# Optimization experiments

Hardware: AMD Instinct MI355X
Metric: run time of the kernel (lower is better)

## Reference

```python
import jax, jax.numpy as jnp
import numpy as np

NEG_SLOPE = 0.01  # F.leaky_relu default


def gcn_layer(h_in, W, b, src, dst, deg_inv_sqrt, n_nodes):
    # GCNConv: linear transform, then symmetric-normalized sum aggregation
    # with self-loops (PyG gcn_norm with add_self_loops=True).
    h = h_in @ W                                   # [N, F_out]
    norm = deg_inv_sqrt[src] * deg_inv_sqrt[dst]   # [E]
    agg = jax.ops.segment_sum(norm[:, None] * h[src], dst, num_segments=n_nodes)
    agg = agg + (deg_inv_sqrt * deg_inv_sqrt)[:, None] * h  # self-loop term (norm = 1/deg)
    return agg + b


def setup_inputs() -> dict:
    key = jax.random.key(0)
    ks = jax.random.split(key, 10)
    N, E = 100000, 3200000
    F_in, H, C = 512, 256, 64
    x = jax.random.normal(ks[0], (N, F_in), dtype=jnp.float32)
    edge_index = jax.random.randint(ks[1], (2, E), 0, N, dtype=jnp.int32)
    dims = [(F_in, H), (H, H), (H, H), (H, C)]
    params = {}
    for i, (fi, fo) in enumerate(dims):
        scale = (1.0 / fi) ** 0.5
        params[f"W{i}"] = jax.random.normal(ks[2 + i], (fi, fo), dtype=jnp.float32) * scale
        params[f"b{i}"] = jnp.zeros((fo,), dtype=jnp.float32)
    return {"x": x, "edge_index": edge_index, **params}


def reference(x, edge_index, W0, b0, W1, b1, W2, b2, W3, b3):
    N = x.shape[0]
    src, dst = edge_index[0], edge_index[1]
    # degree including self-loop (edge weights all 1)
    deg = jax.ops.segment_sum(jnp.ones_like(src, dtype=x.dtype), dst, num_segments=N) + 1.0
    deg_inv_sqrt = jax.lax.rsqrt(deg)
    Ws = [W0, W1, W2, W3]
    bs = [b0, b1, b2, b3]
    h = x
    for i in range(4):
        h = gcn_layer(h, Ws[i], bs[i], src, dst, deg_inv_sqrt, N)
        if i != 3:
            h = jax.nn.leaky_relu(h, NEG_SLOPE)
    return jax.nn.softmax(h, axis=1)
```

## Files before the change

kernel.cpp:

```cpp
#include <hip/hip_runtime.h>
#include <hip/hip_fp16.h>


#define NEG_SLOPE 0.01f

typedef __attribute__((ext_vector_type(8))) _Float16 f16x8;
typedef __attribute__((ext_vector_type(4))) float f32x4;

__device__ inline f16x8 f16x8_zero() {
    f16x8 v;
#pragma unroll
    for (int q = 0; q < 8; ++q) v[q] = (_Float16)0.f;
    return v;
}

__global__ void k_degree(const int* __restrict__ dst, int* __restrict__ cnt, int E) {
    int i = blockIdx.x * 256 + threadIdx.x;
    if (i < E) atomicAdd(&cnt[dst[i]], 1);
}

__global__ void k_dis(const int* __restrict__ cnt, float* __restrict__ dis, int N) {
    int i = blockIdx.x * 256 + threadIdx.x;
    if (i < N) dis[i] = rsqrtf((float)cnt[i] + 1.0f);
}

__global__ void k_scan1(const int* __restrict__ cnt, int* __restrict__ excl,
                        int* __restrict__ partials, int n) {
    __shared__ int tmp[1024];
    int tid = threadIdx.x;
    int i = blockIdx.x * 1024 + tid;
    int v = (i < n) ? cnt[i] : 0;
    tmp[tid] = v;
    __syncthreads();
    for (int off = 1; off < 1024; off <<= 1) {
        int t = (tid >= off) ? tmp[tid - off] : 0;
        __syncthreads();
        tmp[tid] += t;
        __syncthreads();
    }
    if (i < n) excl[i] = tmp[tid] - v;
    if (tid == 1023) partials[blockIdx.x] = tmp[tid];
}

__global__ void k_scan2(int* __restrict__ partials, int n) {
    __shared__ int tmp[1024];
    int tid = threadIdx.x;
    int v = (tid < n) ? partials[tid] : 0;
    tmp[tid] = v;
    __syncthreads();
    for (int off = 1; off < 1024; off <<= 1) {
        int t = (tid >= off) ? tmp[tid - off] : 0;
        __syncthreads();
        tmp[tid] += t;
        __syncthreads();
    }
    if (tid < n) partials[tid] = tmp[tid] - v;
}

__global__ void k_scan3(int* __restrict__ row_ptr, const int* __restrict__ partials,
                        int n, int E) {
    int i = blockIdx.x * 256 + threadIdx.x;
    if (i < n) row_ptr[i] = row_ptr[i] + partials[i >> 10];
    if (i == n) row_ptr[n] = E;
}

__global__ void k_init_bcur(const int* __restrict__ row_ptr, int* __restrict__ bcur,
                            int nbuk) {
    int b = blockIdx.x * 256 + threadIdx.x;
    if (b < nbuk) bcur[b * 16] = row_ptr[b << 7];
}

__global__ void k_bucket_fill(const int* __restrict__ src, const int* __restrict__ dst,
                              int* __restrict__ bcur, int* __restrict__ bpool, int E) {
    int i = blockIdx.x * 256 + threadIdx.x;
    if (i < E) {
        int s = src[i], d = dst[i];
        int b = d >> 7;
        int p = atomicAdd(&bcur[b * 16], 1);
        bpool[p] = (s << 7) | (d & 127);
    }
}

__global__ __launch_bounds__(256) void k_place(const int* __restrict__ bpool,
                                               const int* __restrict__ row_ptr,
                                               int* __restrict__ csr, int N) {
    __shared__ int cur[128];
    int b = blockIdx.x;
    int n0 = b << 7;
    int nn = min(128, N - n0);
    int tid = threadIdx.x;
    if (tid < nn) cur[tid] = row_ptr[n0 + tid];
    __syncthreads();
    int lo = row_ptr[n0];
    int hi = row_ptr[n0 + nn];
    for (int i = lo + tid; i < hi; i += 256) {
        int e = bpool[i];
        int p = atomicAdd(&cur[e & 127], 1);
        csr[p] = e >> 7;
    }
}

__global__ void k_convW(const float* __restrict__ W, _Float16* __restrict__ Wt,
                        int K, int Nf) {
    int gid = blockIdx.x * 256 + threadIdx.x;
    if (gid < K * Nf) {
        int n = gid / K, k = gid - n * K;
        Wt[gid] = (_Float16)W[(size_t)k * Nf + n];
    }
}

template <int BN, bool A_HALF, bool OUT_HALF>
__global__ __launch_bounds__(256) void k_gemm_mfma(const void* __restrict__ Ap,
                                                   const _Float16* __restrict__ Bt,
                                                   void* __restrict__ Cp,
                                                   const float* __restrict__ rowscale,
                                                   int M, int K, int Nf) {
    constexpr int BM = 128, BK = 32;
    constexpr int WAVES_N = (BN == 128) ? 2 : 1;
    constexpr int WAVES_M = 4 / WAVES_N;
    constexpr int WM = BM / (WAVES_M * 16);
    constexpr int WN = BN / (WAVES_N * 16);
    constexpr int LDK = BK + 8;
    __shared__ _Float16 As[BM][LDK];
    __shared__ _Float16 Bs[BN][LDK];

    const int tid = threadIdx.x;
    const int ln = tid & 63, wv = tid >> 6;
    const int wm = wv / WAVES_N, wn = wv % WAVES_N;
    const int rowq = wm * WM * 16, colq = wn * WN * 16;
    const int rowBase = blockIdx.x * BM;
    const int colBase = blockIdx.y * BN;
    const int l15 = ln & 15, lq = ln >> 4;

    f32x4 acc[WM][WN];
#pragma unroll
    for (int i = 0; i < WM; ++i)
#pragma unroll
        for (int j = 0; j < WN; ++j) {
            acc[i][j][0] = 0.f; acc[i][j][1] = 0.f;
            acc[i][j][2] = 0.f; acc[i][j][3] = 0.f;
        }

    constexpr int ASL2 = (BM * BK / 8) / 256;
    constexpr int BSL2 = (BN * BK / 8) / 256;

    for (int kt = 0; kt < K; kt += BK) {
        f16x8 aL[ASL2];
        float4 aF[ASL2][2];
#pragma unroll
        for (int s2 = 0; s2 < ASL2; ++s2) {
            int s = tid + s2 * 256;
            int r = s >> 2, k0 = (s & 3) * 8;
            int gr = rowBase + r;
            if constexpr (A_HALF) {
                aL[s2] = (gr < M)
                    ? *(const f16x8*)((const _Float16*)Ap + (size_t)gr * K + kt + k0)
                    : f16x8_zero();
            } else {
                if (gr < M) {
                    const float* ap = (const float*)Ap + (size_t)gr * K + kt + k0;
                    aF[s2][0] = *(const float4*)ap;
                    aF[s2][1] = *(const float4*)(ap + 4);
                } else {
                    aF[s2][0] = make_float4(0.f, 0.f, 0.f, 0.f);
                    aF[s2][1] = make_float4(0.f, 0.f, 0.f, 0.f);
                }
            }
        }
        f16x8 bL[BSL2];
#pragma unroll
        for (int s2 = 0; s2 < BSL2; ++s2) {
            int s = tid + s2 * 256;
            int n = s >> 2, k0 = (s & 3) * 8;
            bL[s2] = *(const f16x8*)&Bt[(size_t)(colBase + n) * K + kt + k0];
        }
        __syncthreads();
#pragma unroll
        for (int s2 = 0; s2 < ASL2; ++s2) {
            int s = tid + s2 * 256;
            int r = s >> 2, k0 = (s & 3) * 8;
            if constexpr (A_HALF) {
                *(f16x8*)&As[r][k0] = aL[s2];
            } else {
                f16x8 h;
                h[0] = (_Float16)aF[s2][0].x; h[1] = (_Float16)aF[s2][0].y;
                h[2] = (_Float16)aF[s2][0].z; h[3] = (_Float16)aF[s2][0].w;
                h[4] = (_Float16)aF[s2][1].x; h[5] = (_Float16)aF[s2][1].y;
                h[6] = (_Float16)aF[s2][1].z; h[7] = (_Float16)aF[s2][1].w;
                *(f16x8*)&As[r][k0] = h;
            }
        }
#pragma unroll
        for (int s2 = 0; s2 < BSL2; ++s2) {
            int s = tid + s2 * 256;
            int n = s >> 2, k0 = (s & 3) * 8;
            *(f16x8*)&Bs[n][k0] = bL[s2];
        }
        __syncthreads();
        f16x8 af[WM], bf[WN];
#pragma unroll
        for (int i = 0; i < WM; ++i)
            af[i] = *(const f16x8*)&As[rowq + i * 16 + l15][lq * 8];
#pragma unroll
        for (int j = 0; j < WN; ++j)
            bf[j] = *(const f16x8*)&Bs[colq + j * 16 + l15][lq * 8];
#pragma unroll
        for (int i = 0; i < WM; ++i)
#pragma unroll
            for (int j = 0; j < WN; ++j)
                acc[i][j] = __builtin_amdgcn_mfma_f32_16x16x32_f16(af[i], bf[j],
                                                                   acc[i][j], 0, 0, 0);
    }

#pragma unroll
    for (int i = 0; i < WM; ++i) {
#pragma unroll
        for (int r = 0; r < 4; ++r) {
            int row = rowBase + rowq + i * 16 + lq * 4 + r;
            if (row < M) {
                float rs = rowscale[row];
#pragma unroll
                for (int j = 0; j < WN; ++j) {
                    int col = colBase + colq + j * 16 + l15;
                    float v = rs * acc[i][j][r];
                    if constexpr (OUT_HALF)
                        ((_Float16*)Cp)[(size_t)row * Nf + col] = (_Float16)v;
                    else
                        ((float*)Cp)[(size_t)row * Nf + col] = v;
                }
            }
        }
    }
}

__global__ __launch_bounds__(256) void k_agg256_h(const _Float16* __restrict__ H,
                                                  const int* __restrict__ row_ptr,
                                                  const int* __restrict__ csr,
                                                  const float* __restrict__ dis,
                                                  const float* __restrict__ bias,
                                                  _Float16* __restrict__ out, int N) {
    int wave = threadIdx.x >> 6;
    int lane = threadIdx.x & 63;
    int node = blockIdx.x * 4 + wave;
    if (node >= N) return;
    int beg = row_ptr[node], end = row_ptr[node + 1];
    const int half = lane >> 5;
    const int fo = (lane & 31) * 8;

    float acc[8];
#pragma unroll
    for (int q = 0; q < 8; ++q) acc[q] = 0.f;

    int e = beg;
    for (; e + 16 <= end; e += 16) {
        int msrc = csr[e + (lane & 15)];
#pragma unroll
        for (int j = 0; j < 8; ++j) {
            int s = __shfl(msrc, 2 * j + half);
            f16x8 v = *(const f16x8*)(H + (size_t)s * 256 + fo);
#pragma unroll
            for (int q = 0; q < 8; ++q) acc[q] += (float)v[q];
        }
    }
    if (e < end) {
        int n = end - e;
        int idx = e + (lane & 15);
        int msrc = csr[idx < end ? idx : end - 1];
#pragma unroll
        for (int j = 0; j < 8; ++j) {
            int eidx = 2 * j + half;
            if (eidx < n) {
                int s = __shfl(msrc, eidx);
                f16x8 v = *(const f16x8*)(H + (size_t)s * 256 + fo);
#pragma unroll
                for (int q = 0; q < 8; ++q) acc[q] += (float)v[q];
            }
        }
    }

#pragma unroll
    for (int q = 0; q < 8; ++q) acc[q] += __shfl_xor(acc[q], 32);

    float di = dis[node];
    f16x8 sv = *(const f16x8*)(H + (size_t)node * 256 + fo);
    float4 b0 = ((const float4*)bias)[(lane & 31) * 2];
    float4 b1 = ((const float4*)bias)[(lane & 31) * 2 + 1];
    float bb[8] = {b0.x, b0.y, b0.z, b0.w, b1.x, b1.y, b1.z, b1.w};
    f16x8 hh;
#pragma unroll
    for (int q = 0; q < 8; ++q) {
        float r = fmaf(di, acc[q] + (float)sv[q], bb[q]);
        r = r > 0.f ? r : NEG_SLOPE * r;
        hh[q] = (_Float16)r;
    }
    if (half == 0)
        *(f16x8*)(out + (size_t)node * 256 + fo) = hh;
}

__global__ __launch_bounds__(256) void k_agg64_softmax(const _Float16* __restrict__ H,
                                                       const int* __restrict__ row_ptr,
                                                       const int* __restrict__ csr,
                                                       const float* __restrict__ dis,
                                                       const float* __restrict__ bias,
                                                       float* __restrict__ out, int N) {
    int wave = threadIdx.x >> 6;
    int lane = threadIdx.x & 63;
    int node = blockIdx.x * 4 + wave;
    if (node >= N) return;
    int beg = row_ptr[node], end = row_ptr[node + 1];
    const int g = lane >> 3;
    const int fo = (lane & 7) * 8;

    float acc[8];
#pragma unroll
    for (int q = 0; q < 8; ++q) acc[q] = 0.f;

    int e = beg;
    for (; e + 32 <= end; e += 32) {
        int msrc = csr[e + (lane & 31)];
#pragma unroll
        for (int j = 0; j < 4; ++j) {
            int s = __shfl(msrc, 8 * j + g);
            f16x8 v = *(const f16x8*)(H + (size_t)s * 64 + fo);
#pragma unroll
            for (int q = 0; q < 8; ++q) acc[q] += (float)v[q];
        }
    }
    if (e < end) {
        int n = end - e;
        int idx = e + (lane & 31);
        int msrc = csr[idx < end ? idx : end - 1];
#pragma unroll
        for (int j = 0; j < 4; ++j) {
            int eidx = 8 * j + g;
            if (eidx < n) {
                int s = __shfl(msrc, eidx);
                f16x8 v = *(const f16x8*)(H + (size_t)s * 64 + fo);
#pragma unroll
                for (int q = 0; q < 8; ++q) acc[q] += (float)v[q];
            }
        }
    }

#pragma unroll
    for (int q = 0; q < 8; ++q) {
        acc[q] += __shfl_xor(acc[q], 8);
        acc[q] += __shfl_xor(acc[q], 16);
        acc[q] += __shfl_xor(acc[q], 32);
    }

    float di = dis[node];
    f16x8 sv = *(const f16x8*)(H + (size_t)node * 64 + fo);
    float4 b0 = ((const float4*)bias)[(lane & 7) * 2];
    float4 b1 = ((const float4*)bias)[(lane & 7) * 2 + 1];
    float bb[8] = {b0.x, b0.y, b0.z, b0.w, b1.x, b1.y, b1.z, b1.w};
    float v[8];
    float m = -3.4e38f;
#pragma unroll
    for (int q = 0; q < 8; ++q) {
        v[q] = fmaf(di, acc[q] + (float)sv[q], bb[q]);
        m = fmaxf(m, v[q]);
    }
#pragma unroll
    for (int off = 4; off; off >>= 1) m = fmaxf(m, __shfl_xor(m, off));
    float s = 0.f;
    float ex[8];
#pragma unroll
    for (int q = 0; q < 8; ++q) { ex[q] = __expf(v[q] - m); s += ex[q]; }
#pragma unroll
    for (int off = 4; off; off >>= 1) s += __shfl_xor(s, off);
    float inv = 1.f / s;
    if (g == 0) {
        float4 o0 = make_float4(ex[0] * inv, ex[1] * inv, ex[2] * inv, ex[3] * inv);
        float4 o1 = make_float4(ex[4] * inv, ex[5] * inv, ex[6] * inv, ex[7] * inv);
        float* op = out + (size_t)node * 64 + fo;
        *(float4*)op = o0;
        *(float4*)(op + 4) = o1;
    }
}

extern "C" void kernel_launch(void* const* d_in, const int* in_sizes, int n_in,
                              void* d_out, int out_size, void* d_ws, size_t ws_size,
                              hipStream_t stream) {
    const float* x  = (const float*)d_in[0];
    const int*   ei = (const int*)d_in[1];
    const float* W0 = (const float*)d_in[2];
    const float* b0 = (const float*)d_in[3];
    const float* W1 = (const float*)d_in[4];
    const float* b1 = (const float*)d_in[5];
    const float* W2 = (const float*)d_in[6];
    const float* b2 = (const float*)d_in[7];
    const float* W3 = (const float*)d_in[8];
    const float* b3 = (const float*)d_in[9];

    const int N = in_sizes[0] / 512;
    const int E = in_sizes[1] / 2;
    const int* src = ei;
    const int* dst = ei + E;
    const int NBUK = (N + 127) >> 7;

    auto align256 = [](size_t v) { return (v + 255) & ~(size_t)255; };
    char* w = (char*)d_ws;
    _Float16* hA = (_Float16*)w;     w += align256((size_t)N * 256 * 2);
    _Float16* hB = (_Float16*)w;     w += align256((size_t)N * 256 * 2);
    int*   csr = (int*)w;            w += align256((size_t)E * 4);
    int*   bpool = (int*)w;          w += align256((size_t)E * 4);
    int*   cnt = (int*)w;            w += align256((size_t)N * 4);
    float* dis = (float*)w;          w += align256((size_t)N * 4);
    int*   row_ptr = (int*)w;        w += align256((size_t)(N + 1) * 4);
    int*   bcur = (int*)w;           w += align256((size_t)NBUK * 16 * 4);
    int*   partials = (int*)w;       w += align256((size_t)1024 * 4);
    _Float16* Wt0 = (_Float16*)w;    w += align256((size_t)256 * 512 * 2);
    _Float16* Wt1 = (_Float16*)w;    w += align256((size_t)256 * 256 * 2);
    _Float16* Wt2 = (_Float16*)w;    w += align256((size_t)256 * 256 * 2);
    _Float16* Wt3 = (_Float16*)w;    w += align256((size_t)64 * 256 * 2);
    (void)ws_size; (void)n_in; (void)out_size;

    const int nchunks = (N + 1023) / 1024;

    hipMemsetAsync(cnt, 0, (size_t)N * 4, stream);
    k_degree<<<(E + 255) / 256, 256, 0, stream>>>(dst, cnt, E);
    k_dis<<<(N + 255) / 256, 256, 0, stream>>>(cnt, dis, N);
    k_scan1<<<nchunks, 1024, 0, stream>>>(cnt, row_ptr, partials, N);
    k_scan2<<<1, 1024, 0, stream>>>(partials, nchunks);
    k_scan3<<<(N + 1 + 255) / 256, 256, 0, stream>>>(row_ptr, partials, N, E);
    k_init_bcur<<<(NBUK + 255) / 256, 256, 0, stream>>>(row_ptr, bcur, NBUK);
    k_bucket_fill<<<(E + 255) / 256, 256, 0, stream>>>(src, dst, bcur, bpool, E);
    k_place<<<NBUK, 256, 0, stream>>>(bpool, row_ptr, csr, N);

    k_convW<<<(512 * 256 + 255) / 256, 256, 0, stream>>>(W0, Wt0, 512, 256);
    k_convW<<<(256 * 256 + 255) / 256, 256, 0, stream>>>(W1, Wt1, 256, 256);
    k_convW<<<(256 * 256 + 255) / 256, 256, 0, stream>>>(W2, Wt2, 256, 256);
    k_convW<<<(256 * 64 + 255) / 256, 256, 0, stream>>>(W3, Wt3, 256, 64);

    const int gridM = (N + 127) / 128;
    const int nodeBlocks = (N + 3) / 4;

    k_gemm_mfma<128, false, true><<<dim3(gridM, 2), 256, 0, stream>>>(x, Wt0, hA, dis,
                                                                      N, 512, 256);
    k_agg256_h<<<nodeBlocks, 256, 0, stream>>>(hA, row_ptr, csr, dis, b0, hB, N);
    k_gemm_mfma<128, true, true><<<dim3(gridM, 2), 256, 0, stream>>>(hB, Wt1, hA, dis,
                                                                     N, 256, 256);
    k_agg256_h<<<nodeBlocks, 256, 0, stream>>>(hA, row_ptr, csr, dis, b1, hB, N);
    k_gemm_mfma<128, true, true><<<dim3(gridM, 2), 256, 0, stream>>>(hB, Wt2, hA, dis,
                                                                     N, 256, 256);
    k_agg256_h<<<nodeBlocks, 256, 0, stream>>>(hA, row_ptr, csr, dis, b2, hB, N);
    k_gemm_mfma<64, true, true><<<dim3(gridM, 1), 256, 0, stream>>>(hB, Wt3, hA, dis,
                                                                    N, 256, 64);
    k_agg64_softmax<<<nodeBlocks, 256, 0, stream>>>(hA, row_ptr, csr, dis, b3,
                                                    (float*)d_out, N);
}
```

Baseline: 1.493 ms.

## Split 256-wide aggregation into two 128-feature passes for cache locality

Each 256-feature aggregation now runs as two launches, each covering 128 features, and a wave processes four edges at a time with 16 lanes per edge. The goal is to halve the working set of gathered rows per pass so more of the random-access H gathers hit in L2/MALL. In exchange the CSR and row pointers are read twice, there are extra launches, and an extra shuffle-reduction step is needed.

```diff
diff --git a/kernel.cpp b/kernel.cpp
--- a/kernel.cpp
+++ b/kernel.cpp
@@ -238,25 +238,26 @@
                                                   const int* __restrict__ csr,
                                                   const float* __restrict__ dis,
                                                   const float* __restrict__ bias,
-                                                  _Float16* __restrict__ out, int N) {
+                                                  _Float16* __restrict__ out, int N,
+                                                  int foff) {
     int wave = threadIdx.x >> 6;
     int lane = threadIdx.x & 63;
     int node = blockIdx.x * 4 + wave;
     if (node >= N) return;
     int beg = row_ptr[node], end = row_ptr[node + 1];
-    const int half = lane >> 5;
-    const int fo = (lane & 31) * 8;
+    const int q4 = lane >> 4;
+    const int fo = foff + (lane & 15) * 8;
 
     float acc[8];
 #pragma unroll
     for (int q = 0; q < 8; ++q) acc[q] = 0.f;
 
     int e = beg;
-    for (; e + 16 <= end; e += 16) {
-        int msrc = csr[e + (lane & 15)];
+    for (; e + 32 <= end; e += 32) {
+        int msrc = csr[e + (lane & 31)];
 #pragma unroll
         for (int j = 0; j < 8; ++j) {
-            int s = __shfl(msrc, 2 * j + half);
+            int s = __shfl(msrc, 4 * j + q4);
             f16x8 v = *(const f16x8*)(H + (size_t)s * 256 + fo);
 #pragma unroll
             for (int q = 0; q < 8; ++q) acc[q] += (float)v[q];
@@ -264,11 +265,11 @@
     }
     if (e < end) {
         int n = end - e;
-        int idx = e + (lane & 15);
+        int idx = e + (lane & 31);
         int msrc = csr[idx < end ? idx : end - 1];
 #pragma unroll
         for (int j = 0; j < 8; ++j) {
-            int eidx = 2 * j + half;
+            int eidx = 4 * j + q4;
             if (eidx < n) {
                 int s = __shfl(msrc, eidx);
                 f16x8 v = *(const f16x8*)(H + (size_t)s * 256 + fo);
@@ -279,12 +280,16 @@
     }
 
 #pragma unroll
-    for (int q = 0; q < 8; ++q) acc[q] += __shfl_xor(acc[q], 32);
+    for (int q = 0; q < 8; ++q) {
+        acc[q] += __shfl_xor(acc[q], 16);
+        acc[q] += __shfl_xor(acc[q], 32);
+    }
 
     float di = dis[node];
     f16x8 sv = *(const f16x8*)(H + (size_t)node * 256 + fo);
-    float4 b0 = ((const float4*)bias)[(lane & 31) * 2];
-    float4 b1 = ((const float4*)bias)[(lane & 31) * 2 + 1];
+    int b4 = (foff >> 2) + (lane & 15) * 2;
+    float4 b0 = ((const float4*)bias)[b4];
+    float4 b1 = ((const float4*)bias)[b4 + 1];
     float bb[8] = {b0.x, b0.y, b0.z, b0.w, b1.x, b1.y, b1.z, b1.w};
     f16x8 hh;
 #pragma unroll
@@ -293,7 +298,7 @@
         r = r > 0.f ? r : NEG_SLOPE * r;
         hh[q] = (_Float16)r;
     }
-    if (half == 0)
+    if (q4 == 0)
         *(f16x8*)(out + (size_t)node * 256 + fo) = hh;
 }
 
@@ -438,13 +443,16 @@
 
     k_gemm_mfma<128, false, true><<<dim3(gridM, 2), 256, 0, stream>>>(x, Wt0, hA, dis,
                                                                       N, 512, 256);
-    k_agg256_h<<<nodeBlocks, 256, 0, stream>>>(hA, row_ptr, csr, dis, b0, hB, N);
+    k_agg256_h<<<nodeBlocks, 256, 0, stream>>>(hA, row_ptr, csr, dis, b0, hB, N, 0);
+    k_agg256_h<<<nodeBlocks, 256, 0, stream>>>(hA, row_ptr, csr, dis, b0, hB, N, 128);
     k_gemm_mfma<128, true, true><<<dim3(gridM, 2), 256, 0, stream>>>(hB, Wt1, hA, dis,
                                                                      N, 256, 256);
-    k_agg256_h<<<nodeBlocks, 256, 0, stream>>>(hA, row_ptr, csr, dis, b1, hB, N);
+    k_agg256_h<<<nodeBlocks, 256, 0, stream>>>(hA, row_ptr, csr, dis, b1, hB, N, 0);
+    k_agg256_h<<<nodeBlocks, 256, 0, stream>>>(hA, row_ptr, csr, dis, b1, hB, N, 128);
     k_gemm_mfma<128, true, true><<<dim3(gridM, 2), 256, 0, stream>>>(hB, Wt2, hA, dis,
                                                                      N, 256, 256);
-    k_agg256_h<<<nodeBlocks, 256, 0, stream>>>(hA, row_ptr, csr, dis, b2, hB, N);
+    k_agg256_h<<<nodeBlocks, 256, 0, stream>>>(hA, row_ptr, csr, dis, b2, hB, N, 0);
+    k_agg256_h<<<nodeBlocks, 256, 0, stream>>>(hA, row_ptr, csr, dis, b2, hB, N, 128);
     k_gemm_mfma<64, true, true><<<dim3(gridM, 1), 256, 0, stream>>>(hB, Wt3, hA, dis,
                                                                     N, 256, 64);
     k_agg64_softmax<<<nodeBlocks, 256, 0, stream>>>(hA, row_ptr, csr, dis, b3,
```

Result: slower. 1.525 ms (+2.1%).
